# Kernel tuning notes

Measured on AMD Instinct MI355X. Metric: run time of the kernel, lower is better.

The kernel has to match this reference:

```python
import jax, jax.numpy as jnp
import numpy as np

N = 50000   # nodes
E = 800000  # edges per order
F = 128     # input features (== hidden so layers stack)
H = 128     # hidden
C = 10      # classes
L = 3       # num_layers
O = 2       # Order (max_petal_dim)
K = 10      # propagation hops
G = 128     # num graphs in batch
ALPHA = 0.5
EPS = 1e-5  # BatchNorm eps


def _fw_init():
    # HiGCN_prop.reset_parameters: fW[k] = alpha*(1-alpha)^k, fW[K] = (1-alpha)^K
    fw = np.array([ALPHA * (1 - ALPHA) ** k for k in range(K + 1)], dtype=np.float32)
    fw[-1] = (1 - ALPHA) ** K
    return jnp.broadcast_to(jnp.asarray(fw), (L, O, K + 1))


def setup_inputs() -> dict:
    key = jax.random.key(0)
    ks = iter(jax.random.split(key, 64))
    nk = lambda: next(ks)
    s = lambda shape: (jax.random.normal(nk(), shape, jnp.float32) * 0.05)
    x = jax.random.normal(nk(), (N, F), jnp.float32)
    edge_index = jax.random.randint(nk(), (O, 2, E), 0, N, dtype=jnp.int32)
    # scale weights so expected row sum ~0.5 -> stable over K=10 hops
    edge_weight = jax.random.uniform(nk(), (O, E), jnp.float32) * (1.0 / 16.0)
    batch = jnp.sort(jax.random.randint(nk(), (N,), 0, G, dtype=jnp.int32))
    return {
        "x": x, "edge_index": edge_index, "edge_weight": edge_weight, "batch": batch,
        "W_in": s((L, O, F, H)), "b_in": s((L, O, H)),
        "fW": _fw_init(),
        "W_out": s((L, O * H, H)), "b_out": s((L, H)),
        "Wn1": s((L, H, H)), "bn1": s((L, H)), "g1": jnp.ones((L, H), jnp.float32), "be1": s((L, H)),
        "Wn2": s((L, H, H)), "bn2": s((L, H)), "g2": jnp.ones((L, H), jnp.float32), "be2": s((L, H)),
        "W1": s((H, H)), "b1": s((H,)), "W2": s((H, C)), "b2": s((C,)),
    }


def _bn(x, g, b):
    # eval-mode BatchNorm1d: running_mean=0, running_var=1
    return x * (g / jnp.sqrt(1.0 + EPS)) + b


def _spmm(dst, src, w, h):
    # out[dst] += w * h[src]  == matmul(HL, h, reduce='add')
    return jax.ops.segment_sum(w[:, None] * h[src], dst, num_segments=N)


def reference(x, edge_index, edge_weight, batch, W_in, b_in, fW, W_out, b_out,
              Wn1, bn1, g1, be1, Wn2, bn2, g2, be2, W1, b1, W2, b2):
    h = x
    for l in range(L):
        outs = []
        for o in range(O):
            dst, src = edge_index[o, 0], edge_index[o, 1]
            w = edge_weight[o]
            z = h @ W_in[l, o] + b_in[l, o]           # [N, H]
            hid = fW[l, o, 0] * z
            for k in range(K):
                z = _spmm(dst, src, w, z)
                hid = hid + fW[l, o, k + 1] * z
            outs.append(hid)
        xc = jnp.concatenate(outs, axis=1) @ W_out[l] + b_out[l]   # [N, H]
        xc = jnp.maximum(_bn(xc @ Wn1[l] + bn1[l], g1[l], be1[l]), 0.0)
        h = jnp.maximum(_bn(xc @ Wn2[l] + bn2[l], g2[l], be2[l]), 0.0)
    p = jax.ops.segment_sum(h, batch, num_segments=G)              # global_add_pool [G, H]
    p = jnp.maximum(p @ W1 + b1, 0.0)
    return p @ W2 + b2                                             # [G, C]
```

## Files before the change

### kernel.cpp

```cpp
#include <hip/hip_runtime.h>

#define NNODES 50000
#define NEDGES 800000
#define HDIM 128
#define CDIM 10
#define LNUM 3
#define ONUM 2
#define KHOPS 10
#define GNUM 128
#define EPSBN 1e-5f
#define ZPL ((size_t)NNODES * 64)

typedef unsigned int uint;
typedef unsigned short ushort;
typedef __attribute__((ext_vector_type(8))) short bf16x8;
typedef __attribute__((ext_vector_type(4))) float f32x4;

__device__ __forceinline__ ushort f2bf(float f) {
    uint u = __builtin_bit_cast(uint, f);
    uint r = (u + 0x7fffu + ((u >> 16) & 1u)) >> 16;
    return (ushort)r;
}
__device__ __forceinline__ float bf2f_lo(uint u) { return __builtin_bit_cast(float, u << 16); }
__device__ __forceinline__ float bf2f_hi(uint u) { return __builtin_bit_cast(float, u & 0xffff0000u); }

#define KC 128
#define LDA 136
__global__ __launch_bounds__(256) void mfma_gemm(
    const float* __restrict__ A0, const float* __restrict__ A1,
    const ushort* __restrict__ Wt, int Kdim,
    const float* __restrict__ bias, const float* __restrict__ g,
    const float* __restrict__ be, const float* __restrict__ fw0,
    float* __restrict__ outf, ushort* __restrict__ outz,
    float* __restrict__ hid, int relu,
    const ushort* __restrict__ Wt_b, const float* __restrict__ bias_b,
    const float* __restrict__ fw0_b, ushort* __restrict__ outz_b,
    float* __restrict__ hid_b)
{
    if (blockIdx.y) { Wt = Wt_b; bias = bias_b; fw0 = fw0_b; outz = outz_b; hid = hid_b; }
    __shared__ ushort sA[64 * LDA];
    __shared__ ushort sB[128 * LDA];
    const int row0 = blockIdx.x * 64;
    const int tid  = threadIdx.x;
    const int w    = tid >> 6;
    const int lane = tid & 63;
    const int lr   = lane & 15;
    const int q    = lane >> 4;

    f32x4 acc[8];
#pragma unroll
    for (int nt = 0; nt < 8; ++nt)
#pragma unroll
        for (int j = 0; j < 4; ++j) acc[nt][j] = 0.f;

    const int nch = A1 ? 2 : 1;
    for (int c = 0; c < nch; ++c) {
        const float* Asrc = c ? A1 : A0;
        for (int idx = tid; idx < 64 * 64; idx += 256) {
            int r = idx >> 6, kp = idx & 63;
            int row = row0 + r;
            float2 v = make_float2(0.f, 0.f);
            if (row < NNODES) v = ((const float2*)(Asrc + (size_t)row * HDIM))[kp];
            uint pv = (uint)f2bf(v.x) | ((uint)f2bf(v.y) << 16);
            ((uint*)(sA + r * LDA))[kp] = pv;
        }
        for (int idx = tid; idx < 128 * 64; idx += 256) {
            int n = idx >> 6, kp = idx & 63;
            uint u = ((const uint*)(Wt + (size_t)n * Kdim + c * KC))[kp];
            ((uint*)(sB + n * LDA))[kp] = u;
        }
        __syncthreads();
#pragma unroll
        for (int kt = 0; kt < 4; ++kt) {
            bf16x8 a = *(const bf16x8*)(sA + (16 * w + lr) * LDA + kt * 32 + q * 8);
#pragma unroll
            for (int nt = 0; nt < 8; ++nt) {
                bf16x8 b = *(const bf16x8*)(sB + (nt * 16 + lr) * LDA + kt * 32 + q * 8);
                acc[nt] = __builtin_amdgcn_mfma_f32_16x16x32_bf16(a, b, acc[nt], 0, 0, 0);
            }
        }
        __syncthreads();
    }

    const float f0 = fw0 ? fw0[0] : 0.f;
#pragma unroll
    for (int nt = 0; nt < 8; ++nt) {
        int col = nt * 16 + lr;
        float bs = bias[col];
        float sc = 1.f, bt = 0.f;
        if (g) { sc = g[col] * rsqrtf(1.f + EPSBN); bt = be[col]; }
#pragma unroll
        for (int r = 0; r < 4; ++r) {
            int row = row0 + 16 * w + q * 4 + r;
            if (row >= NNODES) continue;
            float v = acc[nt][r] + bs;
            if (g) v = v * sc + bt;
            if (relu) v = fmaxf(v, 0.f);
            if (outf) outf[(size_t)row * HDIM + col] = v;
            if (outz) outz[(size_t)(col >> 6) * ZPL + (size_t)row * 64 + (col & 63)] = f2bf(v);
            if (hid)  hid[(size_t)row * HDIM + col] = f0 * v;
        }
    }
}

__global__ void wtrans_all(const float* __restrict__ W_in, const float* __restrict__ W_out,
                           const float* __restrict__ Wn1, const float* __restrict__ Wn2,
                           ushort* __restrict__ Wt_in, ushort* __restrict__ Wt_out,
                           ushort* __restrict__ Wt_n1, ushort* __restrict__ Wt_n2)
{
    int b = blockIdx.x;
    const float* W; ushort* Wt; int Kd;
    if (b < 6)       { Kd = HDIM;     W = W_in  + (size_t)b * Kd * HDIM;        Wt = Wt_in  + (size_t)b * Kd * HDIM; }
    else if (b < 9)  { Kd = 2 * HDIM; W = W_out + (size_t)(b - 6) * Kd * HDIM;  Wt = Wt_out + (size_t)(b - 6) * Kd * HDIM; }
    else if (b < 12) { Kd = HDIM;     W = Wn1   + (size_t)(b - 9) * Kd * HDIM;  Wt = Wt_n1  + (size_t)(b - 9) * Kd * HDIM; }
    else             { Kd = HDIM;     W = Wn2   + (size_t)(b - 12) * Kd * HDIM; Wt = Wt_n2  + (size_t)(b - 12) * Kd * HDIM; }
    for (int idx = threadIdx.x; idx < Kd * HDIM; idx += 512) {
        int k = idx >> 7, n = idx & 127;
        Wt[(size_t)n * Kd + k] = f2bf(W[idx]);
    }
}

__global__ void gemm_rows(const float* __restrict__ A0,
                          const float* __restrict__ W, const float* __restrict__ bias,
                          float* __restrict__ out, int N, int Hout, int relu)
{
    __shared__ float a[8][HDIM];
    const int row0 = blockIdx.x * 8;
    const int tid  = threadIdx.x;
    for (int r = 0; r < 8; ++r) {
        int row = row0 + r;
        a[r][tid] = (row < N) ? A0[(size_t)row * HDIM + tid] : 0.f;
    }
    __syncthreads();
    if (tid < Hout) {
        float acc[8];
#pragma unroll
        for (int r = 0; r < 8; ++r) acc[r] = 0.f;
        for (int k = 0; k < HDIM; ++k) {
            float wv = W[(size_t)k * Hout + tid];
#pragma unroll
            for (int r = 0; r < 8; ++r) acc[r] += a[r][k] * wv;
        }
        const float bs = bias[tid];
        for (int r = 0; r < 8; ++r) {
            int row = row0 + r;
            if (row >= N) break;
            float v = acc[r] + bs;
            if (relu) v = fmaxf(v, 0.f);
            out[(size_t)row * Hout + tid] = v;
        }
    }
}

__global__ void fill2(const int* __restrict__ ei, const float* __restrict__ ew,
                      int* __restrict__ cnt0, int* __restrict__ cnt1,
                      uint* __restrict__ bk0, uint* __restrict__ bk1)
{
    int e = blockIdx.x * blockDim.x + threadIdx.x;
    if (e >= NEDGES) return;
    int o = blockIdx.y;
    const int* dst = ei + (size_t)o * 2 * NEDGES;
    const int* src = dst + NEDGES;
    float w = ew[(size_t)o * NEDGES + e];
    int d = dst[e];
    int pos = atomicAdd((o ? cnt1 : cnt0) + d, 1);
    if (pos < 64)
        (o ? bk1 : bk0)[((size_t)d << 6) + pos] = ((uint)f2bf(w) << 16) | (uint)src[e];
}

__global__ void spmm2(const int* __restrict__ cnt0, const uint* __restrict__ bk0,
                      const int* __restrict__ cnt1, const uint* __restrict__ bk1,
                      const ushort* __restrict__ zin0, ushort* __restrict__ zout0,
                      const ushort* __restrict__ zin1, ushort* __restrict__ zout1,
                      float* __restrict__ hid0, float* __restrict__ hid1,
                      const float* __restrict__ fw0p, const float* __restrict__ fw1p,
                      int do_hid)
{
    const int o     = blockIdx.y & 1;
    const int plane = blockIdx.y >> 1;
    const int lane  = threadIdx.x & 63;
    const int half  = lane >> 5;
    const int l31   = lane & 31;
    const int node  = blockIdx.x * 8 + ((threadIdx.x >> 6) << 1) + half;
    if (node >= NNODES) return;

    const int*  cnt = o ? cnt1 : cnt0;
    const uint* bk  = o ? bk1 : bk0;
    const uint* zi  = (const uint*)((o ? zin1 : zin0) + plane * ZPL);
    uint*       zo  = (uint*)((o ? zout1 : zout0) + plane * ZPL);
    float*      hid = o ? hid1 : hid0;
    const float* fwp = o ? fw1p : fw0p;

    int n = cnt[node]; n = n > 64 ? 64 : n;
    const uint* b = bk + ((size_t)node << 6);
    float ax = 0.f, ay = 0.f;
    int j = 0;
    for (; j + 3 < n; j += 4) {
        uint e0 = b[j], e1 = b[j + 1], e2 = b[j + 2], e3 = b[j + 3];
        uint u0 = zi[(size_t)(e0 & 0xffffu) * 32 + l31];
        uint u1 = zi[(size_t)(e1 & 0xffffu) * 32 + l31];
        uint u2 = zi[(size_t)(e2 & 0xffffu) * 32 + l31];
        uint u3 = zi[(size_t)(e3 & 0xffffu) * 32 + l31];
        float w0 = bf2f_hi(e0), w1 = bf2f_hi(e1), w2 = bf2f_hi(e2), w3 = bf2f_hi(e3);
        ax += w0 * bf2f_lo(u0) + w1 * bf2f_lo(u1) + w2 * bf2f_lo(u2) + w3 * bf2f_lo(u3);
        ay += w0 * bf2f_hi(u0) + w1 * bf2f_hi(u1) + w2 * bf2f_hi(u2) + w3 * bf2f_hi(u3);
    }
    for (; j < n; ++j) {
        uint e = b[j];
        uint u = zi[(size_t)(e & 0xffffu) * 32 + l31];
        float wt = bf2f_hi(e);
        ax += wt * bf2f_lo(u);
        ay += wt * bf2f_hi(u);
    }
    zo[(size_t)node * 32 + l31] = (uint)f2bf(ax) | ((uint)f2bf(ay) << 16);
    if (do_hid) {
        uint up = zi[(size_t)node * 32 + l31];
        const float c0 = fwp[0], c1 = fwp[1];
        float2* hp = (float2*)hid + (size_t)node * 64 + plane * 32 + l31;
        float2 h = *hp;
        h.x += c0 * bf2f_lo(up) + c1 * ax;
        h.y += c0 * bf2f_hi(up) + c1 * ay;
        *hp = h;
    }
}

__global__ __launch_bounds__(1024) void pool_seg(const float* __restrict__ h,
                                                 const int* __restrict__ batch,
                                                 float* __restrict__ pool)
{
    __shared__ float red[1024];
    const int gph = blockIdx.x;
    const int t  = threadIdx.x & 127;
    const int rr = threadIdx.x >> 7;
    int lo = 0, hi = NNODES;
    while (lo < hi) { int m = (lo + hi) >> 1; if (batch[m] < gph) lo = m + 1; else hi = m; }
    const int beg = lo;
    hi = NNODES;
    while (lo < hi) { int m = (lo + hi) >> 1; if (batch[m] < gph + 1) lo = m + 1; else hi = m; }
    const int end = lo;
    float acc = 0.f;
    for (int i = beg + rr; i < end; i += 8) acc += h[(size_t)i * HDIM + t];
    red[threadIdx.x] = acc;
    __syncthreads();
    if (rr == 0) {
        float s = 0.f;
#pragma unroll
        for (int k = 0; k < 8; ++k) s += red[t + 128 * k];
        pool[(size_t)gph * HDIM + t] = s;
    }
}

extern "C" void kernel_launch(void* const* d_in, const int* in_sizes, int n_in,
                              void* d_out, int out_size, void* d_ws, size_t ws_size,
                              hipStream_t stream)
{
    const float* x     = (const float*)d_in[0];
    const int*   ei    = (const int*)  d_in[1];
    const float* ew    = (const float*)d_in[2];
    const int*   batch = (const int*)  d_in[3];
    const float* W_in  = (const float*)d_in[4];
    const float* b_in  = (const float*)d_in[5];
    const float* fW    = (const float*)d_in[6];
    const float* W_out = (const float*)d_in[7];
    const float* b_out = (const float*)d_in[8];
    const float* Wn1   = (const float*)d_in[9];
    const float* bn1   = (const float*)d_in[10];
    const float* g1    = (const float*)d_in[11];
    const float* be1   = (const float*)d_in[12];
    const float* Wn2   = (const float*)d_in[13];
    const float* bn2   = (const float*)d_in[14];
    const float* g2    = (const float*)d_in[15];
    const float* be2   = (const float*)d_in[16];
    const float* W1    = (const float*)d_in[17];
    const float* b1    = (const float*)d_in[18];
    const float* W2    = (const float*)d_in[19];
    const float* b2    = (const float*)d_in[20];
    float* out = (float*)d_out;

    const size_t NH = (size_t)NNODES * HDIM;
    float* ws  = (float*)d_ws;
    float*  f_A = ws;
    float*  f_B = ws + NH;
    ushort* z0A = (ushort*)(ws + 2 * NH);
    ushort* z0B = z0A + NH;
    ushort* z1A = z0B + NH;
    ushort* z1B = z1A + NH;
    float*  f_pl  = (float*)(z1B + NH);
    float*  f_pl2 = f_pl + (size_t)GNUM * HDIM;

    ushort* Wt_in  = (ushort*)(f_pl2 + (size_t)GNUM * HDIM);
    ushort* Wt_out = Wt_in  + (size_t)6 * HDIM * HDIM;
    ushort* Wt_n1  = Wt_out + (size_t)3 * 2 * HDIM * HDIM;
    ushort* Wt_n2  = Wt_n1  + (size_t)3 * HDIM * HDIM;

    int*  cnt0 = (int*)(Wt_n2 + (size_t)3 * HDIM * HDIM);
    int*  cnt1 = cnt0 + NNODES;
    uint* bk0  = (uint*)(cnt1 + NNODES);
    uint* bk1  = bk0 + ((size_t)NNODES << 6);

    const int gemm_grid = (NNODES + 63) / 64;
    const int edge_grid = (NEDGES + 255) / 256;
    const dim3 spmm_grid((NNODES + 7) / 8, 4);

    wtrans_all<<<15, 512, 0, stream>>>(W_in, W_out, Wn1, Wn2, Wt_in, Wt_out, Wt_n1, Wt_n2);
    hipMemsetAsync(cnt0, 0, 2 * NNODES * sizeof(int), stream);
    fill2<<<dim3(edge_grid, 2), 256, 0, stream>>>(ei, ew, cnt0, cnt1, bk0, bk1);

    const float* curH = x;
    for (int l = 0; l < LNUM; ++l) {
        float* h0 = (curH == (const float*)f_A) ? f_B : f_A;
        float* h1 = (l == 0) ? f_B : (float*)curH;
        const int lo0 = l * ONUM, lo1 = lo0 + 1;
        mfma_gemm<<<dim3(gemm_grid, 2), 256, 0, stream>>>(
            curH, nullptr, Wt_in + (size_t)lo0 * HDIM * HDIM, HDIM,
            b_in + (size_t)lo0 * HDIM, nullptr, nullptr,
            fW + (size_t)lo0 * (KHOPS + 1), nullptr, z0A, h0, 0,
            Wt_in + (size_t)lo1 * HDIM * HDIM, b_in + (size_t)lo1 * HDIM,
            fW + (size_t)lo1 * (KHOPS + 1), z1A, h1);

        ushort *pa0 = z0A, *pb0 = z0B, *pa1 = z1A, *pb1 = z1B;
        for (int k = 1; k <= KHOPS; ++k) {
            spmm2<<<spmm_grid, 256, 0, stream>>>(
                cnt0, bk0, cnt1, bk1, pa0, pb0, pa1, pb1, h0, h1,
                fW + (size_t)lo0 * (KHOPS + 1) + (k - 1),
                fW + (size_t)lo1 * (KHOPS + 1) + (k - 1),
                (k & 1) == 0);
            ushort* t;
            t = pa0; pa0 = pb0; pb0 = t;
            t = pa1; pa1 = pb1; pb1 = t;
        }
        mfma_gemm<<<gemm_grid, 256, 0, stream>>>(
            h0, h1, Wt_out + (size_t)l * 2 * HDIM * HDIM, 2 * HDIM,
            b_out + (size_t)l * HDIM, nullptr, nullptr, nullptr,
            h0, nullptr, nullptr, 0,
            nullptr, nullptr, nullptr, nullptr, nullptr);
        mfma_gemm<<<gemm_grid, 256, 0, stream>>>(
            h0, nullptr, Wt_n1 + (size_t)l * HDIM * HDIM, HDIM,
            bn1 + (size_t)l * HDIM, g1 + (size_t)l * HDIM, be1 + (size_t)l * HDIM,
            nullptr, h1, nullptr, nullptr, 1,
            nullptr, nullptr, nullptr, nullptr, nullptr);
        mfma_gemm<<<gemm_grid, 256, 0, stream>>>(
            h1, nullptr, Wt_n2 + (size_t)l * HDIM * HDIM, HDIM,
            bn2 + (size_t)l * HDIM, g2 + (size_t)l * HDIM, be2 + (size_t)l * HDIM,
            nullptr, h0, nullptr, nullptr, 1,
            nullptr, nullptr, nullptr, nullptr, nullptr);
        curH = h0;
    }

    pool_seg<<<GNUM, 1024, 0, stream>>>(curH, batch, f_pl);
    gemm_rows<<<(GNUM + 7) / 8, 128, 0, stream>>>(f_pl,  W1, b1, f_pl2, GNUM, HDIM, 1);
    gemm_rows<<<(GNUM + 7) / 8, 128, 0, stream>>>(f_pl2, W2, b2, out,   GNUM, CDIM, 0);
}
```

Baseline: 3.078 ms.

## Use row-major bf16 feature layout with one wavefront per node in SpMM

Switches the bf16 propagated-feature buffer from two 64-column planes to a single row-major 128-column layout, so each SpMM node is handled by a full 64-lane wavefront that covers all 128 features. Each bucket entry is now read once per node instead of once per plane, and each gathered neighbor row is one contiguous 256-byte read. Edge bucket entries are also loaded as a single uint4 per group of four. The trade-off is that the planar split no longer keeps a smaller working set per pass for cache locality.

```diff
diff --git a/kernel.cpp b/kernel.cpp
--- a/kernel.cpp
+++ b/kernel.cpp
@@ -9,7 +9,6 @@
 #define KHOPS 10
 #define GNUM 128
 #define EPSBN 1e-5f
-#define ZPL ((size_t)NNODES * 64)
 
 typedef unsigned int uint;
 typedef unsigned short ushort;
@@ -96,9 +95,10 @@
             float v = acc[nt][r] + bs;
             if (g) v = v * sc + bt;
             if (relu) v = fmaxf(v, 0.f);
-            if (outf) outf[(size_t)row * HDIM + col] = v;
-            if (outz) outz[(size_t)(col >> 6) * ZPL + (size_t)row * 64 + (col & 63)] = f2bf(v);
-            if (hid)  hid[(size_t)row * HDIM + col] = f0 * v;
+            size_t off = (size_t)row * HDIM + col;
+            if (outf) outf[off] = v;
+            if (outz) outz[off] = f2bf(v);
+            if (hid)  hid[off]  = f0 * v;
         }
     }
 }
@@ -176,18 +176,14 @@
                       const float* __restrict__ fw0p, const float* __restrict__ fw1p,
                       int do_hid)
 {
-    const int o     = blockIdx.y & 1;
-    const int plane = blockIdx.y >> 1;
-    const int lane  = threadIdx.x & 63;
-    const int half  = lane >> 5;
-    const int l31   = lane & 31;
-    const int node  = blockIdx.x * 8 + ((threadIdx.x >> 6) << 1) + half;
+    const int node = blockIdx.x * 4 + (threadIdx.x >> 6);
     if (node >= NNODES) return;
-
+    const int o    = blockIdx.y;
+    const int lane = threadIdx.x & 63;
     const int*  cnt = o ? cnt1 : cnt0;
     const uint* bk  = o ? bk1 : bk0;
-    const uint* zi  = (const uint*)((o ? zin1 : zin0) + plane * ZPL);
-    uint*       zo  = (uint*)((o ? zout1 : zout0) + plane * ZPL);
+    const uint* zi  = (const uint*)(o ? zin1 : zin0);
+    uint*       zo  = (uint*)(o ? zout1 : zout0);
     float*      hid = o ? hid1 : hid0;
     const float* fwp = o ? fw1p : fw0p;
 
@@ -196,27 +192,28 @@
     float ax = 0.f, ay = 0.f;
     int j = 0;
     for (; j + 3 < n; j += 4) {
-        uint e0 = b[j], e1 = b[j + 1], e2 = b[j + 2], e3 = b[j + 3];
-        uint u0 = zi[(size_t)(e0 & 0xffffu) * 32 + l31];
-        uint u1 = zi[(size_t)(e1 & 0xffffu) * 32 + l31];
-        uint u2 = zi[(size_t)(e2 & 0xffffu) * 32 + l31];
-        uint u3 = zi[(size_t)(e3 & 0xffffu) * 32 + l31];
-        float w0 = bf2f_hi(e0), w1 = bf2f_hi(e1), w2 = bf2f_hi(e2), w3 = bf2f_hi(e3);
+        uint4 e4 = *(const uint4*)(b + j);
+        uint u0 = zi[(size_t)(e4.x & 0xffffu) * 64 + lane];
+        uint u1 = zi[(size_t)(e4.y & 0xffffu) * 64 + lane];
+        uint u2 = zi[(size_t)(e4.z & 0xffffu) * 64 + lane];
+        uint u3 = zi[(size_t)(e4.w & 0xffffu) * 64 + lane];
+        float w0 = bf2f_hi(e4.x), w1 = bf2f_hi(e4.y);
+        float w2 = bf2f_hi(e4.z), w3 = bf2f_hi(e4.w);
         ax += w0 * bf2f_lo(u0) + w1 * bf2f_lo(u1) + w2 * bf2f_lo(u2) + w3 * bf2f_lo(u3);
         ay += w0 * bf2f_hi(u0) + w1 * bf2f_hi(u1) + w2 * bf2f_hi(u2) + w3 * bf2f_hi(u3);
     }
     for (; j < n; ++j) {
         uint e = b[j];
-        uint u = zi[(size_t)(e & 0xffffu) * 32 + l31];
+        uint u = zi[(size_t)(e & 0xffffu) * 64 + lane];
         float wt = bf2f_hi(e);
         ax += wt * bf2f_lo(u);
         ay += wt * bf2f_hi(u);
     }
-    zo[(size_t)node * 32 + l31] = (uint)f2bf(ax) | ((uint)f2bf(ay) << 16);
+    zo[(size_t)node * 64 + lane] = (uint)f2bf(ax) | ((uint)f2bf(ay) << 16);
     if (do_hid) {
-        uint up = zi[(size_t)node * 32 + l31];
+        uint up = zi[(size_t)node * 64 + lane];
         const float c0 = fwp[0], c1 = fwp[1];
-        float2* hp = (float2*)hid + (size_t)node * 64 + plane * 32 + l31;
+        float2* hp = (float2*)hid + (size_t)node * 64 + lane;
         float2 h = *hp;
         h.x += c0 * bf2f_lo(up) + c1 * ax;
         h.y += c0 * bf2f_hi(up) + c1 * ay;
@@ -300,7 +297,7 @@
 
     const int gemm_grid = (NNODES + 63) / 64;
     const int edge_grid = (NEDGES + 255) / 256;
-    const dim3 spmm_grid((NNODES + 7) / 8, 4);
+    const dim3 spmm_grid((NNODES + 3) / 4, 2);
 
     wtrans_all<<<15, 512, 0, stream>>>(W_in, W_out, Wn1, Wn2, Wt_in, Wt_out, Wt_n1, Wt_n2);
     hipMemsetAsync(cnt0, 0, 2 * NNODES * sizeof(int), stream);
```

New measurement: 2.896 ms. -5.9%, faster.
